# Kernel optimization log

Measured on AMD Instinct MI355X. Metric: run time of the kernel, lower is better.

The kernel has to match this reference:

```python
import jax, jax.numpy as jnp
import numpy as np
from jax import lax

K = 3          # spline order
G = 5          # grid intervals
R0, R1 = -4.0, 4.0  # grid_range
IN, HID, OUT = 32, 128, 16
BATCH, SEQ = 256, 512


def make_grid(n_in):
    # extended knot vector: G+2K+1 knots per input, uniform spacing h
    h = (R1 - R0) / G
    knots = R0 + h * jnp.arange(-K, G + K + 1, dtype=jnp.float32)  # [G+2K+1]
    return jnp.broadcast_to(knots, (n_in, G + 2 * K + 1))


def b_splines(x, grid):
    # Cox-de Boor recursion. x: [B, n], grid: [n, G+2K+1] -> basis [B, n, G+K]
    xg = x[..., None]
    B = ((xg >= grid[:, :-1]) & (xg < grid[:, 1:])).astype(x.dtype)
    for d in range(1, K + 1):
        B = ((xg - grid[:, :-(d + 1)]) / (grid[:, d:-1] - grid[:, :-(d + 1)]) * B[..., :-1]
             + (grid[:, d + 1:] - xg) / (grid[:, d + 1:] - grid[:, 1:-d]) * B[..., 1:])
    return B


def kan_layer(x, coef, scale_base, scale_sp, grid):
    # y[b,o] = sum_i scale_base[i,o]*silu(x[b,i]) + scale_sp[i,o]*spline_io(x[b,i])
    base = jax.nn.silu(x)                               # [B, n_in]
    Bsp = b_splines(x, grid)                            # [B, n_in, G+K]
    spline = jnp.einsum('bik,iok->bio', Bsp, coef)      # [B, n_in, n_out]
    return (jnp.einsum('bi,io->bo', base, scale_base)
            + jnp.einsum('bio,io->bo', spline, scale_sp))


def setup_inputs() -> dict:
    key = jax.random.key(0)
    ks = jax.random.split(key, 7)
    x = jax.random.normal(ks[0], (BATCH, SEQ, IN), dtype=jnp.float32)
    coef1 = jax.random.normal(ks[1], (IN + HID, HID, G + K), dtype=jnp.float32) * 0.1
    sb1 = jax.random.normal(ks[2], (IN + HID, HID), dtype=jnp.float32) * 0.05
    sp1 = jax.random.normal(ks[3], (IN + HID, HID), dtype=jnp.float32) * 0.05
    coef2 = jax.random.normal(ks[4], (HID, OUT, G + K), dtype=jnp.float32) * 0.1
    sb2 = jax.random.normal(ks[5], (HID, OUT), dtype=jnp.float32) * 0.05
    sp2 = jax.random.normal(ks[6], (HID, OUT), dtype=jnp.float32) * 0.05
    return {"x": x, "coef1": coef1, "sb1": sb1, "sp1": sp1,
            "coef2": coef2, "sb2": sb2, "sp2": sp2}


def reference(x, coef1, sb1, sp1, coef2, sb2, sp2):
    grid1 = make_grid(IN + HID)
    grid2 = make_grid(HID)

    def step(h, x_t):
        combined = jnp.concatenate([x_t, h], axis=1)        # [B, IN+HID]
        h_new = kan_layer(combined, coef1, sb1, sp1, grid1)  # [B, HID]
        out_t = kan_layer(h_new, coef2, sb2, sp2, grid2)     # [B, OUT]
        return h_new, out_t

    h0 = jnp.zeros((x.shape[0], HID), dtype=x.dtype)
    _, outs = lax.scan(step, h0, jnp.swapaxes(x, 0, 1))  # outs: [T, B, OUT]
    # original stacks all timestep outputs then returns outputs[:, -1, :]
    return outs[-1]
```

## Files before the change

kernel.cpp:

```cpp
#include <hip/hip_runtime.h>
#include <hip/hip_bf16.h>

#define NIN 32
#define NHID 128
#define NOUT 16
#define NIN1 160
#define SEQT 512
#define NB 256

typedef __attribute__((ext_vector_type(8))) short s16x8;
typedef __attribute__((ext_vector_type(4))) float f32x4;

__device__ __forceinline__ unsigned int f2bfbits(float f) {
    unsigned int u = __float_as_uint(f);
    return (u + 0x7fffu + ((u >> 16) & 1u)) >> 16;
}
__device__ __forceinline__ unsigned int packbf(float lo, float hi) {
    return f2bfbits(lo) | (f2bfbits(hi) << 16);
}

__device__ __forceinline__ void spline_feat(float c, float* out4, int* jst) {
    const float t0 = -8.8f, inv_h = 0.625f;
    float u  = (c - t0) * inv_h;
    float uf = floorf(u);
    int   m0 = (int)uf;
    bool valid = (m0 >= 0) && (m0 <= 10);
    float f   = u - uf;
    float omf = 1.0f - f;
    float f2 = f * f, f3 = f2 * f;
    float omf3 = omf * omf * omf;
    const float c6 = 0.16666667f;
    float v0 = omf3 * c6;
    float v1 = __builtin_fmaf(3.0f, f3, __builtin_fmaf(-6.0f, f2, 4.0f)) * c6;
    float v2 = __builtin_fmaf(-3.0f, f3, __builtin_fmaf(3.0f, f + f2, 1.0f)) * c6;
    float v3 = f3 * c6;
    float v[4] = {v0, v1, v2, v3};
    int jb = m0 - 3;
    int js = jb < 0 ? 0 : (jb > 4 ? 4 : jb);
    int sh = js - jb;
    #pragma unroll
    for (int r = 0; r < 4; ++r) {
        int rs = r + sh;
        out4[r] = (valid && rs >= 0 && rs <= 3) ? v[rs] : 0.f;
    }
    *jst = js;
}

__device__ __forceinline__ float fsilu(float c) {
    return c * __builtin_amdgcn_rcpf(1.f + __expf(-c));
}

#define R20(X) X(0) X(1) X(2) X(3) X(4) X(5) X(6) X(7) X(8) X(9) \
               X(10) X(11) X(12) X(13) X(14) X(15) X(16) X(17) X(18) X(19)
#define O8(X) X(0) X(1) X(2) X(3) X(4) X(5) X(6) X(7)
#define K5(X) X(0) X(1) X(2) X(3) X(4)

__attribute__((amdgpu_waves_per_eu(2, 2)))
__global__ void __launch_bounds__(512)
kan_seq(const float* __restrict__ x,
        const float* __restrict__ coef1,
        const float* __restrict__ sb1,
        const float* __restrict__ sp1,
        const float* __restrict__ coef2,
        const float* __restrict__ sb2,
        const float* __restrict__ sp2,
        float* __restrict__ out)
{
    __shared__ __align__(16) unsigned int Fb[NIN1][4];
    __shared__ float Fsil[NIN1];
    __shared__ __align__(16) float red[8][NHID];
    __shared__ float redb[4][NHID];
    __shared__ float Hf[NHID][9];

    const int tid  = threadIdx.x;
    const int b    = blockIdx.x;
    const int lane = tid & 63;
    const int w    = tid >> 6;
    const int o    = tid & 127;
    const int seg  = tid >> 7;
    const int arow = lane & 15;
    const int agrp = lane >> 4;

#define DECLW(k) uint4 wf##k##_0, wf##k##_1, wf##k##_2, wf##k##_3, \
                       wf##k##_4, wf##k##_5, wf##k##_6, wf##k##_7;
    K5(DECLW)
#undef DECLW

#define INITW1(k,t) { \
    int rec = (w * 5 + (k)) * 4 + agrp; \
    int oo  = (t) * 16 + arow; \
    const float4* cp = (const float4*)(coef1 + (size_t)(rec * NHID + oo) * 8); \
    float sp = sp1[rec * NHID + oo]; \
    float4 c0 = cp[0], c1 = cp[1]; \
    wf##k##_##t = make_uint4(packbf(sp * c0.x, sp * c0.y), packbf(sp * c0.z, sp * c0.w), \
                             packbf(sp * c1.x, sp * c1.y), packbf(sp * c1.z, sp * c1.w)); }
#define INITWK(k) INITW1(k,0) INITW1(k,1) INITW1(k,2) INITW1(k,3) \
                  INITW1(k,4) INITW1(k,5) INITW1(k,6) INITW1(k,7)
    K5(INITWK)
#undef INITWK
#undef INITW1

#define DECLSB(p) unsigned int sbp##p;
    R20(DECLSB)
#undef DECLSB
#define INITSB(p) { int iA = seg * 40 + 2 * (p); \
    sbp##p = packbf(sb1[iA * NHID + o], sb1[(iA + 1) * NHID + o]); }
    R20(INITSB)
#undef INITSB

    ((float*)red)[tid] = 0.f;
    ((float*)red)[tid + 512] = 0.f;
    ((float*)redb)[tid] = 0.f;
    float xv = (tid < NIN) ? x[(size_t)b * SEQT * NIN + tid] : 0.f;
    __syncthreads();

    const int fbase = w * 20 + agrp;

    for (int t = 0; t < SEQT; ++t) {
        if (tid < NIN1) {
            float c;
            if (tid < NIN) c = xv;
            else {
                int hi = tid - NIN;
                c = ((red[0][hi] + red[1][hi]) + (red[2][hi] + red[3][hi]))
                  + ((red[4][hi] + red[5][hi]) + (red[6][hi] + red[7][hi]))
                  + ((redb[0][hi] + redb[1][hi]) + (redb[2][hi] + redb[3][hi]));
            }
            Fsil[tid] = fsilu(c);
            float b4[4]; int js;
            spline_feat(c, b4, &js);
            float e[8];
            #pragma unroll
            for (int k = 0; k < 8; ++k) {
                int d = k - js;
                e[k] = (d >= 0 && d < 4) ? b4[d] : 0.f;
            }
            uint4 pk;
            pk.x = packbf(e[0], e[1]); pk.y = packbf(e[2], e[3]);
            pk.z = packbf(e[4], e[5]); pk.w = packbf(e[6], e[7]);
            *(uint4*)&Fb[tid][0] = pk;
        }
        if (tid < NIN) {
            int tn = (t + 1 < SEQT) ? (t + 1) : t;
            xv = x[((size_t)b * SEQT + tn) * NIN + tid];
        }
        __syncthreads();

        uint4 bq0 = *(const uint4*)&Fb[fbase][0];
        uint4 bq1 = *(const uint4*)&Fb[fbase + 4][0];

        float vsil = Fsil[seg * 40 + (lane < 40 ? lane : 0)];
        float bc0 = 0.f, bc1 = 0.f;
#define DOTB(p) { \
        float sb_lo = __uint_as_float(sbp##p << 16); \
        float sb_hi = __uint_as_float(sbp##p & 0xffff0000u); \
        float slA = __int_as_float(__builtin_amdgcn_readlane(__float_as_int(vsil), 2 * (p))); \
        float slB = __int_as_float(__builtin_amdgcn_readlane(__float_as_int(vsil), 2 * (p) + 1)); \
        bc0 = __builtin_fmaf(slA, sb_lo, bc0); \
        bc1 = __builtin_fmaf(slB, sb_hi, bc1); }
        R20(DOTB)
#undef DOTB
        redb[seg][o] = bc0 + bc1;

#define DECLAC(t) f32x4 ac##t = {0.f, 0.f, 0.f, 0.f};
        O8(DECLAC)
#undef DECLAC
#define MMROW(k, bqv) { s16x8 bb_ = __builtin_bit_cast(s16x8, bqv); \
        ac0 = __builtin_amdgcn_mfma_f32_16x16x32_bf16(__builtin_bit_cast(s16x8, wf##k##_0), bb_, ac0, 0, 0, 0); \
        ac1 = __builtin_amdgcn_mfma_f32_16x16x32_bf16(__builtin_bit_cast(s16x8, wf##k##_1), bb_, ac1, 0, 0, 0); \
        ac2 = __builtin_amdgcn_mfma_f32_16x16x32_bf16(__builtin_bit_cast(s16x8, wf##k##_2), bb_, ac2, 0, 0, 0); \
        ac3 = __builtin_amdgcn_mfma_f32_16x16x32_bf16(__builtin_bit_cast(s16x8, wf##k##_3), bb_, ac3, 0, 0, 0); \
        ac4 = __builtin_amdgcn_mfma_f32_16x16x32_bf16(__builtin_bit_cast(s16x8, wf##k##_4), bb_, ac4, 0, 0, 0); \
        ac5 = __builtin_amdgcn_mfma_f32_16x16x32_bf16(__builtin_bit_cast(s16x8, wf##k##_5), bb_, ac5, 0, 0, 0); \
        ac6 = __builtin_amdgcn_mfma_f32_16x16x32_bf16(__builtin_bit_cast(s16x8, wf##k##_6), bb_, ac6, 0, 0, 0); \
        ac7 = __builtin_amdgcn_mfma_f32_16x16x32_bf16(__builtin_bit_cast(s16x8, wf##k##_7), bb_, ac7, 0, 0, 0); }
        MMROW(0, bq0)  uint4 bq2 = *(const uint4*)&Fb[fbase + 8][0];
        MMROW(1, bq1)  uint4 bq3 = *(const uint4*)&Fb[fbase + 12][0];
        MMROW(2, bq2)  uint4 bq4 = *(const uint4*)&Fb[fbase + 16][0];
        MMROW(3, bq3)
        MMROW(4, bq4)
#undef MMROW

#define WRR(t) if ((lane & 15) == (t)) \
            *(f32x4*)&red[w][(t) * 16 + (agrp << 2)] = ac##t;
        O8(WRR)
#undef WRR
        __syncthreads();
    }

    if (tid < NHID) {
        float c = ((red[0][tid] + red[1][tid]) + (red[2][tid] + red[3][tid]))
                + ((red[4][tid] + red[5][tid]) + (red[6][tid] + red[7][tid]))
                + ((redb[0][tid] + redb[1][tid]) + (redb[2][tid] + redb[3][tid]));
        float sil = fsilu(c);
        float b4[4]; int js;
        spline_feat(c, b4, &js);
        #pragma unroll
        for (int k = 0; k < 8; ++k) {
            int d = k - js;
            Hf[tid][k] = (d >= 0 && d < 4) ? b4[d] : 0.f;
        }
        Hf[tid][8] = sil;
    }
    __syncthreads();
    if (tid < 128) {
        int o2 = tid & 15, isg = tid >> 4;
        float acc = 0.f;
        for (int q = 0; q < 16; ++q) {
            int i = isg * 16 + q;
            const float* c2 = coef2 + (size_t)(i * NOUT + o2) * 8;
            float s = 0.f;
            #pragma unroll
            for (int k = 0; k < 8; ++k) s += Hf[i][k] * c2[k];
            acc += Hf[i][8] * sb2[i * NOUT + o2] + sp2[i * NOUT + o2] * s;
        }
        ((float*)red)[isg * 16 + o2] = acc;
    }
    __syncthreads();
    if (tid < NOUT) {
        float a = 0.f;
        #pragma unroll
        for (int g = 0; g < 8; ++g) a += ((float*)red)[g * 16 + tid];
        out[(size_t)b * NOUT + tid] = a;
    }
}

extern "C" void kernel_launch(void* const* d_in, const int* in_sizes, int n_in,
                              void* d_out, int out_size, void* d_ws, size_t ws_size,
                              hipStream_t stream) {
    kan_seq<<<NB, 512, 0, stream>>>(
        (const float*)d_in[0], (const float*)d_in[1], (const float*)d_in[2],
        (const float*)d_in[3], (const float*)d_in[4], (const float*)d_in[5],
        (const float*)d_in[6], (float*)d_out);
}
```

Baseline: 1.036 ms.

## Compute per-wave features locally and double-buffer partials to drop a barrier

Each wave now builds the spline and SiLU features for its own 20 input rows in registers and in wave-private scratch. Before, a block-wide feature buffer was filled and then read by all waves. The base-weight dot product is reassigned per wave over its own inputs, and the reduction partials are double-buffered across timesteps. This removes one __syncthreads per recurrent step. In exchange, every wave redundantly reads 16 partial sums per hidden feature, and the schedule relies on a manual lgkmcnt wait plus a sched_barrier.

Result: slower. 1.070 ms (+3.3%).

```diff
diff --git a/kernel.cpp b/kernel.cpp
--- a/kernel.cpp
+++ b/kernel.cpp
@@ -52,6 +52,8 @@
 
 #define R20(X) X(0) X(1) X(2) X(3) X(4) X(5) X(6) X(7) X(8) X(9) \
                X(10) X(11) X(12) X(13) X(14) X(15) X(16) X(17) X(18) X(19)
+#define R10A(X) X(0) X(1) X(2) X(3) X(4) X(5) X(6) X(7) X(8) X(9)
+#define R10B(X) X(10) X(11) X(12) X(13) X(14) X(15) X(16) X(17) X(18) X(19)
 #define O8(X) X(0) X(1) X(2) X(3) X(4) X(5) X(6) X(7)
 #define K5(X) X(0) X(1) X(2) X(3) X(4)
 
@@ -66,20 +68,17 @@
         const float* __restrict__ sp2,
         float* __restrict__ out)
 {
-    __shared__ __align__(16) unsigned int Fb[NIN1][4];
-    __shared__ float Fsil[NIN1];
-    __shared__ __align__(16) float red[8][NHID];
-    __shared__ float redb[4][NHID];
+    __shared__ __align__(16) unsigned int scr[8][20][4];
+    __shared__ __align__(16) float part[2][16][NHID];
     __shared__ float Hf[NHID][9];
 
     const int tid  = threadIdx.x;
     const int b    = blockIdx.x;
     const int lane = tid & 63;
     const int w    = tid >> 6;
-    const int o    = tid & 127;
-    const int seg  = tid >> 7;
     const int arow = lane & 15;
     const int agrp = lane >> 4;
+    const int rec20 = w * 20 + lane;
 
 #define DECLW(k) uint4 wf##k##_0, wf##k##_1, wf##k##_2, wf##k##_3, \
                        wf##k##_4, wf##k##_5, wf##k##_6, wf##k##_7;
@@ -103,30 +102,38 @@
 #define DECLSB(p) unsigned int sbp##p;
     R20(DECLSB)
 #undef DECLSB
-#define INITSB(p) { int iA = seg * 40 + 2 * (p); \
-    sbp##p = packbf(sb1[iA * NHID + o], sb1[(iA + 1) * NHID + o]); }
+#define INITSB(p) { int i = w * 20 + (p); \
+    sbp##p = packbf(sb1[i * NHID + lane], sb1[i * NHID + lane + 64]); }
     R20(INITSB)
 #undef INITSB
 
-    ((float*)red)[tid] = 0.f;
-    ((float*)red)[tid + 512] = 0.f;
-    ((float*)redb)[tid] = 0.f;
-    float xv = (tid < NIN) ? x[(size_t)b * SEQT * NIN + tid] : 0.f;
+    #pragma unroll
+    for (int z = 0; z < 8; ++z) ((float*)part)[tid + 512 * z] = 0.f;
+    float xv = 0.f;
+    if (lane < 20 && rec20 < NIN) xv = x[(size_t)b * SEQT * NIN + rec20];
     __syncthreads();
 
-    const int fbase = w * 20 + agrp;
-
     for (int t = 0; t < SEQT; ++t) {
-        if (tid < NIN1) {
+        const int rb = t & 1, wb = rb ^ 1;
+
+        float xv_use = xv;
+        if (lane < 20 && rec20 < NIN) {
+            int tn = (t + 1 < SEQT) ? (t + 1) : t;
+            xv = x[((size_t)b * SEQT + tn) * NIN + rec20];
+        }
+        float silu_f = 0.f;
+        if (lane < 20) {
             float c;
-            if (tid < NIN) c = xv;
+            if (rec20 < NIN) c = xv_use;
             else {
-                int hi = tid - NIN;
-                c = ((red[0][hi] + red[1][hi]) + (red[2][hi] + red[3][hi]))
-                  + ((red[4][hi] + red[5][hi]) + (red[6][hi] + red[7][hi]))
-                  + ((redb[0][hi] + redb[1][hi]) + (redb[2][hi] + redb[3][hi]));
+                int hi = rec20 - NIN;
+                float s0 = (part[rb][0][hi] + part[rb][1][hi]) + (part[rb][2][hi] + part[rb][3][hi]);
+                float s1 = (part[rb][4][hi] + part[rb][5][hi]) + (part[rb][6][hi] + part[rb][7][hi]);
+                float s2 = (part[rb][8][hi] + part[rb][9][hi]) + (part[rb][10][hi] + part[rb][11][hi]);
+                float s3 = (part[rb][12][hi] + part[rb][13][hi]) + (part[rb][14][hi] + part[rb][15][hi]);
+                c = (s0 + s1) + (s2 + s3);
             }
-            Fsil[tid] = fsilu(c);
+            silu_f = fsilu(c);
             float b4[4]; int js;
             spline_feat(c, b4, &js);
             float e[8];
@@ -138,33 +145,32 @@
             uint4 pk;
             pk.x = packbf(e[0], e[1]); pk.y = packbf(e[2], e[3]);
             pk.z = packbf(e[4], e[5]); pk.w = packbf(e[6], e[7]);
-            *(uint4*)&Fb[tid][0] = pk;
-        }
-        if (tid < NIN) {
-            int tn = (t + 1 < SEQT) ? (t + 1) : t;
-            xv = x[((size_t)b * SEQT + tn) * NIN + tid];
-        }
-        __syncthreads();
-
-        uint4 bq0 = *(const uint4*)&Fb[fbase][0];
-        uint4 bq1 = *(const uint4*)&Fb[fbase + 4][0];
-
-        float vsil = Fsil[seg * 40 + (lane < 40 ? lane : 0)];
-        float bc0 = 0.f, bc1 = 0.f;
+            *(uint4*)&scr[w][lane][0] = pk;
+        }
+
+        float bc_a = 0.f, bc_b = 0.f;
 #define DOTB(p) { \
         float sb_lo = __uint_as_float(sbp##p << 16); \
         float sb_hi = __uint_as_float(sbp##p & 0xffff0000u); \
-        float slA = __int_as_float(__builtin_amdgcn_readlane(__float_as_int(vsil), 2 * (p))); \
-        float slB = __int_as_float(__builtin_amdgcn_readlane(__float_as_int(vsil), 2 * (p) + 1)); \
-        bc0 = __builtin_fmaf(slA, sb_lo, bc0); \
-        bc1 = __builtin_fmaf(slB, sb_hi, bc1); }
-        R20(DOTB)
+        float slr = __int_as_float(__builtin_amdgcn_readlane(__float_as_int(silu_f), (p))); \
+        bc_a = __builtin_fmaf(slr, sb_lo, bc_a); \
+        bc_b = __builtin_fmaf(slr, sb_hi, bc_b); }
+        R10A(DOTB)
+
+        asm volatile("s_waitcnt lgkmcnt(0)" ::: "memory");
+        __builtin_amdgcn_sched_barrier(0);
+        uint4 bq0 = *(const uint4*)&scr[w][agrp][0];
+        uint4 bq1 = *(const uint4*)&scr[w][4 + agrp][0];
+
+        R10B(DOTB)
 #undef DOTB
-        redb[seg][o] = bc0 + bc1;
-
-#define DECLAC(t) f32x4 ac##t = {0.f, 0.f, 0.f, 0.f};
-        O8(DECLAC)
-#undef DECLAC
+        part[wb][8 + w][lane] = bc_a;
+        part[wb][8 + w][lane + 64] = bc_b;
+
+        f32x4 ac0 = {0.f,0.f,0.f,0.f}, ac1 = {0.f,0.f,0.f,0.f},
+              ac2 = {0.f,0.f,0.f,0.f}, ac3 = {0.f,0.f,0.f,0.f},
+              ac4 = {0.f,0.f,0.f,0.f}, ac5 = {0.f,0.f,0.f,0.f},
+              ac6 = {0.f,0.f,0.f,0.f}, ac7 = {0.f,0.f,0.f,0.f};
 #define MMROW(k, bqv) { s16x8 bb_ = __builtin_bit_cast(s16x8, bqv); \
         ac0 = __builtin_amdgcn_mfma_f32_16x16x32_bf16(__builtin_bit_cast(s16x8, wf##k##_0), bb_, ac0, 0, 0, 0); \
         ac1 = __builtin_amdgcn_mfma_f32_16x16x32_bf16(__builtin_bit_cast(s16x8, wf##k##_1), bb_, ac1, 0, 0, 0); \
@@ -174,24 +180,26 @@
         ac5 = __builtin_amdgcn_mfma_f32_16x16x32_bf16(__builtin_bit_cast(s16x8, wf##k##_5), bb_, ac5, 0, 0, 0); \
         ac6 = __builtin_amdgcn_mfma_f32_16x16x32_bf16(__builtin_bit_cast(s16x8, wf##k##_6), bb_, ac6, 0, 0, 0); \
         ac7 = __builtin_amdgcn_mfma_f32_16x16x32_bf16(__builtin_bit_cast(s16x8, wf##k##_7), bb_, ac7, 0, 0, 0); }
-        MMROW(0, bq0)  uint4 bq2 = *(const uint4*)&Fb[fbase + 8][0];
-        MMROW(1, bq1)  uint4 bq3 = *(const uint4*)&Fb[fbase + 12][0];
-        MMROW(2, bq2)  uint4 bq4 = *(const uint4*)&Fb[fbase + 16][0];
+        MMROW(0, bq0)  uint4 bq2 = *(const uint4*)&scr[w][8 + agrp][0];
+        MMROW(1, bq1)  uint4 bq3 = *(const uint4*)&scr[w][12 + agrp][0];
+        MMROW(2, bq2)  uint4 bq4 = *(const uint4*)&scr[w][16 + agrp][0];
         MMROW(3, bq3)
         MMROW(4, bq4)
 #undef MMROW
 
-#define WRR(t) if ((lane & 15) == (t)) \
-            *(f32x4*)&red[w][(t) * 16 + (agrp << 2)] = ac##t;
+#define WRR(tt) if ((lane & 15) == (tt)) \
+            *(f32x4*)&part[wb][w][(tt) * 16 + (agrp << 2)] = ac##tt;
         O8(WRR)
 #undef WRR
         __syncthreads();
     }
 
     if (tid < NHID) {
-        float c = ((red[0][tid] + red[1][tid]) + (red[2][tid] + red[3][tid]))
-                + ((red[4][tid] + red[5][tid]) + (red[6][tid] + red[7][tid]))
-                + ((redb[0][tid] + redb[1][tid]) + (redb[2][tid] + redb[3][tid]));
+        float s0 = (part[0][0][tid] + part[0][1][tid]) + (part[0][2][tid] + part[0][3][tid]);
+        float s1 = (part[0][4][tid] + part[0][5][tid]) + (part[0][6][tid] + part[0][7][tid]);
+        float s2 = (part[0][8][tid] + part[0][9][tid]) + (part[0][10][tid] + part[0][11][tid]);
+        float s3 = (part[0][12][tid] + part[0][13][tid]) + (part[0][14][tid] + part[0][15][tid]);
+        float c = (s0 + s1) + (s2 + s3);
         float sil = fsilu(c);
         float b4[4]; int js;
         spline_feat(c, b4, &js);
@@ -214,13 +222,13 @@
             for (int k = 0; k < 8; ++k) s += Hf[i][k] * c2[k];
             acc += Hf[i][8] * sb2[i * NOUT + o2] + sp2[i * NOUT + o2] * s;
         }
-        ((float*)red)[isg * 16 + o2] = acc;
+        ((float*)part)[isg * 16 + o2] = acc;
     }
     __syncthreads();
     if (tid < NOUT) {
         float a = 0.f;
         #pragma unroll
-        for (int g = 0; g < 8; ++g) a += ((float*)red)[g * 16 + tid];
+        for (int g = 0; g < 8; ++g) a += ((float*)part)[g * 16 + tid];
         out[(size_t)b * NOUT + tid] = a;
     }
 }
```
